# Kernel optimization log

Hardware: AMD Instinct MI355X
Metric: run time of the kernel (lower is better)

## Reference

```python
import jax, jax.numpy as jnp
import numpy as np

N = 8192
TEMP = 0.5
EPS = 1e-12


def _normalize(z):
    # F.normalize(z, p=2, dim=1): x / max(||x||, eps)
    n = jnp.sqrt(jnp.sum(z * z, axis=1, keepdims=True))
    return z / jnp.maximum(n, EPS)


def _gcn(edge_index, edge_weight, x, w, b):
    # torch.sparse.mm(adj, x @ w): out[row] += adj[row, col] * support[col]
    support = x @ w
    msg = support[edge_index[1]] * edge_weight[:, None]
    return jax.ops.segment_sum(msg, edge_index[0], num_segments=N) + b


def _encoder(edge_index, edge_weight, feat, w_l1a, b_l1a, w_l1b, b_l1b, w_g1, b_g1, w_g2, b_g2):
    x = jax.nn.relu(feat @ w_l1a + b_l1a) @ w_l1b + b_l1b  # [N, 32]
    h = jax.nn.relu(_gcn(edge_index, edge_weight, x, w_g1, b_g1))  # [N, hid]
    return _gcn(edge_index, edge_weight, h, w_g2, b_g2)  # [N, act_fn]


def _proj(h, w_fc1, b_fc1, w_fc2, b_fc2):
    return jax.nn.elu(h @ w_fc1 + b_fc1) @ w_fc2 + b_fc2


def _loss(z1, z2):
    z1n = _normalize(z1)
    z2n = _normalize(z2)
    refl = jnp.exp((z1n @ z1n.T) / TEMP)      # [N, N]
    between = jnp.exp((z1n @ z2n.T) / TEMP)   # [N, N]
    denom = refl.sum(1) + between.sum(1) - jnp.diagonal(refl)
    return -jnp.log(jnp.diagonal(between) / denom)


def setup_inputs() -> dict:
    key = jax.random.key(0)
    ks = jax.random.split(key, 20)
    E = 262144
    in_dim, hid_dim, act_fn, out_dim = 512, 256, 128, 64

    def kaiming(k, shape):
        fan_in = shape[0]
        bound = np.sqrt(6.0 / fan_in)
        return jax.random.uniform(k, shape, jnp.float32, -bound, bound)

    return {
        "feat1": jax.random.normal(ks[0], (N, in_dim), jnp.float32),
        "feat2": jax.random.normal(ks[1], (N, in_dim), jnp.float32),
        "edge_index1": jax.random.randint(ks[2], (2, E), 0, N, jnp.int32),
        "edge_weight1": jax.random.uniform(ks[3], (E,), jnp.float32),
        "edge_index2": jax.random.randint(ks[4], (2, E), 0, N, jnp.int32),
        "edge_weight2": jax.random.uniform(ks[5], (E,), jnp.float32),
        "w_l1a": kaiming(ks[6], (in_dim, 64)),
        "b_l1a": jnp.zeros((64,), jnp.float32),
        "w_l1b": kaiming(ks[7], (64, 32)),
        "b_l1b": jnp.zeros((32,), jnp.float32),
        "w_g1": kaiming(ks[8], (32, hid_dim)),
        "b_g1": jnp.zeros((hid_dim,), jnp.float32),
        "w_g2": kaiming(ks[9], (hid_dim, act_fn)),
        "b_g2": jnp.zeros((act_fn,), jnp.float32),
        "w_fc1": kaiming(ks[10], (act_fn, out_dim)),
        "b_fc1": jnp.zeros((out_dim,), jnp.float32),
        "w_fc2": kaiming(ks[11], (out_dim, act_fn)),
        "b_fc2": jnp.zeros((act_fn,), jnp.float32),
    }


def reference(feat1, feat2, edge_index1, edge_weight1, edge_index2, edge_weight2,
              w_l1a, b_l1a, w_l1b, b_l1b, w_g1, b_g1, w_g2, b_g2,
              w_fc1, b_fc1, w_fc2, b_fc2):
    h1 = _encoder(edge_index1, edge_weight1, feat1, w_l1a, b_l1a, w_l1b, b_l1b, w_g1, b_g1, w_g2, b_g2)
    h2 = _encoder(edge_index2, edge_weight2, feat2, w_l1a, b_l1a, w_l1b, b_l1b, w_g1, b_g1, w_g2, b_g2)
    z1 = _proj(h1, w_fc1, b_fc1, w_fc2, b_fc2)
    z2 = _proj(h2, w_fc1, b_fc1, w_fc2, b_fc2)
    l1 = _loss(z1, z2)
    l2 = _loss(z2, z1)
    return ((l1 + l2) * 0.5).mean()
```

## Files before the change

### kernel.cpp

```cpp
#include <hip/hip_runtime.h>
#include <hip/hip_bf16.h>
#include <math.h>


#define NROWS 8192
#define MROWS 16384
#define NEDGE 262144

typedef __attribute__((ext_vector_type(8))) short bf16x8;
typedef __attribute__((ext_vector_type(4))) float f32x4;
typedef __attribute__((ext_vector_type(2))) float f32x2;
typedef __attribute__((ext_vector_type(8))) int i32x8;
typedef long long i64;

__device__ __forceinline__ short f2bf(float f){
  union { float f; unsigned u; } cv; cv.f = f;
  unsigned u = cv.u;
  unsigned r = (u + 0x7fffu + ((u >> 16) & 1u)) >> 16;
  return (short)r;
}
__device__ __forceinline__ f32x4 mfma16(bf16x8 a, bf16x8 b, f32x4 c){
  return __builtin_amdgcn_mfma_f32_16x16x32_bf16(a, b, c, 0, 0, 0);
}
__device__ __forceinline__ float fexp2(float x){
#if __has_builtin(__builtin_amdgcn_exp2f)
  return __builtin_amdgcn_exp2f(x);
#else
  return exp2f(x);
#endif
}

template<int CTRL>
__device__ __forceinline__ float dpp_add(float v){
  int s = __builtin_amdgcn_update_dpp(0, __builtin_bit_cast(int, v),
                                      CTRL, 0xf, 0xf, true);
  return v + __builtin_bit_cast(float, s);
}
__device__ __forceinline__ float red16(float v){
  v = dpp_add<0x101>(v);
  v = dpp_add<0x102>(v);
  v = dpp_add<0x104>(v);
  v = dpp_add<0x108>(v);
  return v;
}

__device__ unsigned char f2e4m3_sw(float f){
  float a = fabsf(f);
  unsigned s = (__float_as_uint(f)>>24)&0x80u;
  if (!(a>0.f)) return (unsigned char)s;
  if (a>448.f) a=448.f;
  int e; frexpf(a,&e);
  int eff=e-1;
  unsigned code;
  if (eff<-6){
    float q=rintf(a*512.f);
    code=(unsigned)q; if(code>7)code=7;
  } else {
    float q=rintf(a*exp2f((float)(3-eff)));
    unsigned mant=(unsigned)q;
    if(mant>=16){mant=8;eff++;}
    if(eff>8) return (unsigned char)(s|0x7e);
    code=((unsigned)(eff+7)<<3)|(mant-8);
  }
  return (unsigned char)(s|code);
}
__device__ __forceinline__ unsigned short pack2fp8(float a, float b){
#if __has_builtin(__builtin_amdgcn_cvt_pk_fp8_f32)
  int v = __builtin_amdgcn_cvt_pk_fp8_f32(a, b, 0, false);
  return (unsigned short)(v & 0xffff);
#else
  return (unsigned short)((unsigned)f2e4m3_sw(a) | ((unsigned)f2e4m3_sw(b)<<8));
#endif
}

struct WtArgs {
  const float* src[6];
  short* dst[6];
  int K[6], N[6];
  int off[7];
  int nwt;
};
__global__ void setup_k(WtArgs a, const int* __restrict__ ei1, const int* __restrict__ ei2,
                        int* __restrict__ deg1, int* __restrict__ deg2){
  int b = blockIdx.x;
  if (b < a.nwt){
    int i = b*256 + threadIdx.x;
    if (i >= a.off[6]) return;
    int s = 0;
    #pragma unroll
    for (int j=1;j<6;j++) if (i >= a.off[j]) s=j;
    int l = i - a.off[s];
    int K=a.K[s], N=a.N[s];
    int k=l/N, n=l-k*N;
    a.dst[s][(long)n*K+k] = f2bf(a.src[s][l]);
  } else {
    int hb = b - a.nwt;
    const int* ei = (hb < NEDGE/256) ? ei1 : ei2;
    int* deg = (hb < NEDGE/256) ? deg1 : deg2;
    int e = (hb % (NEDGE/256))*256 + threadIdx.x;
    atomicAdd(&deg[ei[e]], 1);
  }
}

__global__ __launch_bounds__(256) void mlp12_k(const float* __restrict__ F0, const float* __restrict__ F1,
                                               const short* __restrict__ Wa, const float* __restrict__ ba,
                                               const short* __restrict__ Wb, const float* __restrict__ bb,
                                               short* __restrict__ xb){
  __shared__ short As[32*520];
  __shared__ short a1s[32*72];
  const int tid = threadIdx.x;
  const int m0 = blockIdx.x*32;
  const float* F = (m0 < NROWS) ? (F0 + (long)m0*512) : (F1 + (long)(m0-NROWS)*512);
  {
    float4 st[16];
    #pragma unroll
    for (int i=0;i<16;i++) st[i] = *(const float4*)(F + (long)(i*256+tid)*4);
    #pragma unroll
    for (int i=0;i<16;i++){
      int idx = i*256+tid, row = idx>>7, c4 = idx&127;
      unsigned lo = (unsigned)(unsigned short)f2bf(st[i].x) | ((unsigned)(unsigned short)f2bf(st[i].y)<<16);
      unsigned hi = (unsigned)(unsigned short)f2bf(st[i].z) | ((unsigned)(unsigned short)f2bf(st[i].w)<<16);
      uint2 o = {lo, hi};
      *(uint2*)&As[row*520 + c4*4] = o;
    }
  }
  __syncthreads();
  const int wave = tid>>6, lane = tid&63, quad = lane>>4, cl = lane&15;
  f32x4 zero = {0.f,0.f,0.f,0.f};
  {
    const int wno = wave*16;
    f32x4 acc[2] = {zero, zero};
    #pragma unroll
    for (int kc=0;kc<16;kc++){
      const int ko = kc*32 + quad*8;
      bf16x8 a0 = *(const bf16x8*)&As[(cl)*520 + ko];
      bf16x8 a1 = *(const bf16x8*)&As[(16+cl)*520 + ko];
      bf16x8 b = *(const bf16x8*)(Wa + (long)(wno + cl)*512 + ko);
      acc[0] = mfma16(a0, b, acc[0]);
      acc[1] = mfma16(a1, b, acc[1]);
    }
    int col = wno + cl;
    float bv = ba[col];
    #pragma unroll
    for (int mt=0;mt<2;mt++)
      #pragma unroll
      for (int r=0;r<4;r++)
        a1s[(mt*16 + quad*4 + r)*72 + col] = f2bf(fmaxf(acc[mt][r] + bv, 0.f));
  }
  __syncthreads();
  if (wave < 2){
    f32x4 acc2[2] = {zero, zero};
    #pragma unroll
    for (int kc=0;kc<2;kc++){
      const int ko = kc*32 + quad*8;
      bf16x8 a = *(const bf16x8*)&a1s[(wave*16+cl)*72 + ko];
      #pragma unroll
      for (int nt=0;nt<2;nt++){
        bf16x8 b = *(const bf16x8*)(Wb + (long)(nt*16 + cl)*64 + ko);
        acc2[nt] = mfma16(a, b, acc2[nt]);
      }
    }
    #pragma unroll
    for (int nt=0;nt<2;nt++){
      int col = nt*16 + cl;
      float bv = bb[col];
      #pragma unroll
      for (int r=0;r<4;r++)
        xb[(long)(m0 + wave*16 + quad*4 + r)*32 + col] = f2bf(acc2[nt][r] + bv);
    }
  }
}

__global__ void scan2_k(const int* __restrict__ deg1, int* __restrict__ rs1, int* __restrict__ cur1,
                        const int* __restrict__ deg2, int* __restrict__ rs2, int* __restrict__ cur2){
  const int* deg = blockIdx.x ? deg2 : deg1;
  int* rowstart = blockIdx.x ? rs2 : rs1;
  int* cursor = blockIdx.x ? cur2 : cur1;
  __shared__ int csum[256];
  int t = threadIdx.x;
  int loc[32];
  int s = 0;
  for (int j=0;j<32;j++){ int d = deg[t*32+j]; loc[j] = s; s += d; }
  int v = s;
  csum[t] = v;
  __syncthreads();
  for (int st=1; st<256; st<<=1){
    int o = (t >= st) ? csum[t-st] : 0;
    __syncthreads();
    v += o;
    csum[t] = v;
    __syncthreads();
  }
  int base = v - s;
  for (int j=0;j<32;j++){ int w = base + loc[j]; rowstart[t*32+j]=w; cursor[t*32+j]=w; }
  if (t==255) rowstart[NROWS] = v;
}
__global__ void fill2_k(const int* __restrict__ ei1, const float* __restrict__ w1, int* __restrict__ cur1,
                        int* __restrict__ ecol1, float* __restrict__ ew1,
                        const int* __restrict__ ei2, const float* __restrict__ w2, int* __restrict__ cur2,
                        int* __restrict__ ecol2, float* __restrict__ ew2){
  int b = blockIdx.x;
  bool g2 = (b >= NEDGE/256);
  const int* ei = g2 ? ei2 : ei1;
  const float* w = g2 ? w2 : w1;
  int* cursor = g2 ? cur2 : cur1;
  int* ecol = g2 ? ecol2 : ecol1;
  float* ew = g2 ? ew2 : ew1;
  int e = (b % (NEDGE/256))*256 + threadIdx.x;
  int r = ei[e];
  int p = atomicAdd(&cursor[r], 1);
  ecol[p] = ei[NEDGE + e];
  ew[p] = w[e];
}

__device__ __forceinline__ void acc8(float* acc, int4 v, float f){
  const unsigned* u = (const unsigned*)&v;
  #pragma unroll
  for (int i=0;i<4;i++){
    union{unsigned x; float y;} lo, hi;
    lo.x = u[i] << 16;
    hi.x = u[i] & 0xffff0000u;
    acc[2*i]   = fmaf(f, lo.y, acc[2*i]);
    acc[2*i+1] = fmaf(f, hi.y, acc[2*i+1]);
  }
}
template<int C>
__device__ __forceinline__ void gather_row(float* acc, const short* sb,
                                           const int* ec, const float* w, int s, int e){
  int k = s;
  for (; k+16 <= e; k+=16){
    int c[16]; float f[16]; int4 v[16];
    #pragma unroll
    for (int u=0;u<16;u++){ c[u]=ec[k+u]; f[u]=w[k+u]; }
    #pragma unroll
    for (int u=0;u<16;u++) v[u] = *(const int4*)(sb + (long)c[u]*C);
    #pragma unroll
    for (int u=0;u<16;u++) acc8(acc, v[u], f[u]);
  }
  for (; k+4 <= e; k+=4){
    int c0=ec[k],c1=ec[k+1],c2=ec[k+2],c3=ec[k+3];
    float f0=w[k],f1=w[k+1],f2=w[k+2],f3=w[k+3];
    int4 v0 = *(const int4*)(sb + (long)c0*C);
    int4 v1 = *(const int4*)(sb + (long)c1*C);
    int4 v2 = *(const int4*)(sb + (long)c2*C);
    int4 v3 = *(const int4*)(sb + (long)c3*C);
    acc8(acc,v0,f0); acc8(acc,v1,f1); acc8(acc,v2,f2); acc8(acc,v3,f3);
  }
  for (; k < e; k++){
    int4 v0 = *(const int4*)(sb + (long)ec[k]*C);
    acc8(acc,v0,w[k]);
  }
}

template<int C, bool RELU, bool HASB>
__global__ __launch_bounds__(256) void gather_k(const short* __restrict__ sup,
    const int* __restrict__ rs1, const int* __restrict__ ec1, const float* __restrict__ w1,
    const int* __restrict__ rs2, const int* __restrict__ ec2, const float* __restrict__ w2,
    const float* __restrict__ bias, short* __restrict__ out){
  constexpr int G = C/8;
  const int g = threadIdx.x % G;
  const int sub = threadIdx.x / G;
  const int row = blockIdx.x*(256/G) + sub;
  const int* rs; const int* ec; const float* w; int soff, lr;
  if (row < NROWS){ rs=rs1; ec=ec1; w=w1; soff=0; lr=row; }
  else            { rs=rs2; ec=ec2; w=w2; soff=NROWS; lr=row-NROWS; }
  const short* sb = sup + (long)soff*C + g*8;
  float acc[8];
  #pragma unroll
  for (int j=0;j<8;j++) acc[j] = HASB ? bias[g*8+j] : 0.f;
  gather_row<C>(acc, sb, ec, w, rs[lr], rs[lr+1]);
  int4 ov;
  unsigned* ou = (unsigned*)&ov;
  #pragma unroll
  for (int i=0;i<4;i++){
    float a0 = acc[2*i], a1 = acc[2*i+1];
    if (RELU){ a0 = fmaxf(a0,0.f); a1 = fmaxf(a1,0.f); }
    ou[i] = (unsigned)(unsigned short)f2bf(a0) | ((unsigned)(unsigned short)f2bf(a1)<<16);
  }
  *(int4*)(out + (long)row*C + g*8) = ov;
}

__global__ __launch_bounds__(256) void gg_k(const short* __restrict__ xb,
    const int* __restrict__ rs1, const int* __restrict__ ec1, const float* __restrict__ w1,
    const int* __restrict__ rs2, const int* __restrict__ ec2, const float* __restrict__ w2,
    const short* __restrict__ Wg1, const float* __restrict__ bg1,
    const short* __restrict__ Wg2, short* __restrict__ s2){
  __shared__ short axs[64*40];
  __shared__ short hbs[64*264];
  const int tid = threadIdx.x;
  const int m0 = blockIdx.x*64;
  {
    const int g = tid & 3, sub = tid >> 2;
    const int row = m0 + sub;
    const int* rs; const int* ec; const float* w; int soff, lr;
    if (row < NROWS){ rs=rs1; ec=ec1; w=w1; soff=0; lr=row; }
    else            { rs=rs2; ec=ec2; w=w2; soff=NROWS; lr=row-NROWS; }
    const short* sb = xb + (long)soff*32 + g*8;
    float acc[8];
    #pragma unroll
    for (int j=0;j<8;j++) acc[j] = 0.f;
    gather_row<32>(acc, sb, ec, w, rs[lr], rs[lr+1]);
    int4 ov;
    unsigned* ou = (unsigned*)&ov;
    #pragma unroll
    for (int i=0;i<4;i++)
      ou[i] = (unsigned)(unsigned short)f2bf(acc[2*i]) | ((unsigned)(unsigned short)f2bf(acc[2*i+1])<<16);
    *(int4*)&axs[sub*40 + g*8] = ov;
  }
  __syncthreads();
  const int wave = tid>>6, lane = tid&63, quad = lane>>4, cl = lane&15;
  f32x4 zero = {0.f,0.f,0.f,0.f};
  {
    const int wno = wave*64;
    f32x4 acc[4][4];
    #pragma unroll
    for (int i=0;i<4;i++)
      #pragma unroll
      for (int j=0;j<4;j++) acc[i][j]=zero;
    const int ko = quad*8;
    bf16x8 a[4], b[4];
    #pragma unroll
    for (int mt=0;mt<4;mt++)
      a[mt] = *(const bf16x8*)&axs[(mt*16+cl)*40 + ko];
    #pragma unroll
    for (int nt=0;nt<4;nt++)
      b[nt] = *(const bf16x8*)(Wg1 + (long)(wno + nt*16 + cl)*32 + ko);
    #pragma unroll
    for (int mt=0;mt<4;mt++)
      #pragma unroll
      for (int nt=0;nt<4;nt++)
        acc[mt][nt] = mfma16(a[mt], b[nt], acc[mt][nt]);
    #pragma unroll
    for (int nt=0;nt<4;nt++){
      int col = wno + nt*16 + cl;
      float bv = bg1[col];
      #pragma unroll
      for (int mt=0;mt<4;mt++)
        #pragma unroll
        for (int r=0;r<4;r++)
          hbs[(mt*16 + quad*4 + r)*264 + col] = f2bf(fmaxf(acc[mt][nt][r] + bv, 0.f));
    }
  }
  __syncthreads();
  {
    const int wno = wave*32;
    f32x4 acc[4][2];
    #pragma unroll
    for (int i=0;i<4;i++){ acc[i][0]=zero; acc[i][1]=zero; }
    #pragma unroll
    for (int kc=0;kc<8;kc++){
      const int ko = kc*32 + quad*8;
      bf16x8 a[4], b[2];
      #pragma unroll
      for (int mt=0;mt<4;mt++)
        a[mt] = *(const bf16x8*)&hbs[(mt*16+cl)*264 + ko];
      #pragma unroll
      for (int nt=0;nt<2;nt++)
        b[nt] = *(const bf16x8*)(Wg2 + (long)(wno + nt*16 + cl)*256 + ko);
      #pragma unroll
      for (int mt=0;mt<4;mt++)
        #pragma unroll
        for (int nt=0;nt<2;nt++)
          acc[mt][nt] = mfma16(a[mt], b[nt], acc[mt][nt]);
    }
    #pragma unroll
    for (int mt=0;mt<4;mt++)
      #pragma unroll
      for (int nt=0;nt<2;nt++){
        int col = wno + nt*16 + cl;
        #pragma unroll
        for (int r=0;r<4;r++)
          s2[(long)(m0 + mt*16 + quad*4 + r)*128 + col] = f2bf(acc[mt][nt][r]);
      }
  }
}

__global__ __launch_bounds__(256) void pn_k(const short* __restrict__ hh,
    const short* __restrict__ Wf1, const float* __restrict__ bf1,
    const short* __restrict__ Wf2, const float* __restrict__ bf2,
    unsigned short* __restrict__ Zf, float* __restrict__ bdot){
  __shared__ short hs[64*136];
  __shared__ short t2s[64*72];
  __shared__ float zs[64*132];
  __shared__ float sp[4][64];
  __shared__ float dp[4][32];
  __shared__ float rnS[64];
  const float SQKE = 1.6986436f;
  const int tid = threadIdx.x;
  const int wave = tid>>6, lane = tid&63, quad = lane>>4, cl = lane&15;
  const int m0h = blockIdx.x*32;
  {
    const short* r1 = hh + (long)m0h*128;
    const short* r2 = hh + (long)(NROWS + m0h)*128;
    #pragma unroll
    for (int i=0;i<2;i++){
      int idx = i*256 + tid;
      int row = idx >> 4, c16 = idx & 15;
      *(int4*)&hs[row*136 + c16*8] = *(const int4*)(r1 + row*128 + c16*8);
      *(int4*)&hs[(32+row)*136 + c16*8] = *(const int4*)(r2 + row*128 + c16*8);
    }
  }
  __syncthreads();
  f32x4 zero = {0.f,0.f,0.f,0.f};
  {
    const int wno = wave*16;
    f32x4 acc[4];
    #pragma unroll
    for (int i=0;i<4;i++) acc[i]=zero;
    #pragma unroll
    for (int kc=0;kc<4;kc++){
      const int ko = kc*32 + quad*8;
      bf16x8 a[4], b;
      #pragma unroll
      for (int mt=0;mt<4;mt++)
        a[mt] = *(const bf16x8*)&hs[(mt*16+cl)*136 + ko];
      b = *(const bf16x8*)(Wf1 + (long)(wno + cl)*128 + ko);
      #pragma unroll
      for (int mt=0;mt<4;mt++) acc[mt] = mfma16(a[mt], b, acc[mt]);
    }
    int col = wno + cl;
    float bv = bf1[col];
    #pragma unroll
    for (int mt=0;mt<4;mt++)
      #pragma unroll
      for (int r=0;r<4;r++){
        float v = acc[mt][r] + bv;
        v = (v > 0.f) ? v : expm1f(v);
        t2s[(mt*16 + quad*4 + r)*72 + col] = f2bf(v);
      }
  }
  __syncthreads();
  {
    const int wno = wave*32;
    f32x4 acc[4][2];
    #pragma unroll
    for (int i=0;i<4;i++){ acc[i][0]=zero; acc[i][1]=zero; }
    #pragma unroll
    for (int kc=0;kc<2;kc++){
      const int ko = kc*32 + quad*8;
      bf16x8 a[4], b[2];
      #pragma unroll
      for (int mt=0;mt<4;mt++)
        a[mt] = *(const bf16x8*)&t2s[(mt*16+cl)*72 + ko];
      #pragma unroll
      for (int nt=0;nt<2;nt++)
        b[nt] = *(const bf16x8*)(Wf2 + (long)(wno + nt*16 + cl)*64 + ko);
      #pragma unroll
      for (int mt=0;mt<4;mt++)
        #pragma unroll
        for (int nt=0;nt<2;nt++)
          acc[mt][nt] = mfma16(a[mt], b[nt], acc[mt][nt]);
    }
    #pragma unroll
    for (int mt=0;mt<4;mt++)
      #pragma unroll
      for (int nt=0;nt<2;nt++){
        int col = wno + nt*16 + cl;
        float bv = bf2[col];
        #pragma unroll
        for (int r=0;r<4;r++)
          zs[(mt*16 + quad*4 + r)*132 + col] = acc[mt][nt][r] + bv;
      }
  }
  __syncthreads();
  {
    int row = tid & 63, qtr = tid >> 6;
    const float* zr = &zs[row*132 + qtr*32];
    float s = 0.f;
    #pragma unroll 8
    for (int c=0;c<32;c++) s += zr[c]*zr[c];
    sp[qtr][row] = s;
    if (row < 32){
      const float* zb_ = &zs[(row+32)*132 + qtr*32];
      float d = 0.f;
      #pragma unroll 8
      for (int c=0;c<32;c++) d += zr[c]*zb_[c];
      dp[qtr][row] = d;
    }
  }
  __syncthreads();
  if (tid < 64){
    float ssq = sp[0][tid]+sp[1][tid]+sp[2][tid]+sp[3][tid];
    rnS[tid] = 1.f / fmaxf(sqrtf(ssq), 1e-12f);
  }
  __syncthreads();
  if (tid < 32){
    float dot = dp[0][tid]+dp[1][tid]+dp[2][tid]+dp[3][tid];
    bdot[m0h + tid] = dot * rnS[tid] * rnS[tid+32];
  }
  {
    int lr = tid >> 2;
    int grow = (lr < 32) ? (m0h + lr) : (NROWS + m0h + lr - 32);
    float s = rnS[lr] * SQKE;
    int p0 = (tid & 3)*16;
    long gbase = (long)(grow>>4)*1024 + (long)(grow&15)*16 + (long)(p0>>4)*256;
    #pragma unroll
    for (int pp=0;pp<16;pp++){
      int p = p0 + pp;
      Zf[gbase + pp] = pack2fp8(zs[lr*132 + 2*p]*s, zs[lr*132 + 2*p + 1]*s);
    }
  }
}

__global__ __launch_bounds__(256,4) void gram3_k(const unsigned char* __restrict__ Zf,
                                                 float* __restrict__ P){
  __shared__ float srow[4][64];
  __shared__ float scol[4][64];
  const int wave = threadIdx.x>>6, lane = threadIdx.x&63;
  const int t = blockIdx.x*4 + wave;
  int ti = (int)((513.0f - sqrtf(513.0f*513.0f - 8.0f*(float)t))*0.5f);
  while ((ti+1)*256 - ((ti+1)*ti)/2 <= t) ti++;
  while (ti*256 - (ti*(ti-1))/2 > t) ti--;
  const int tj = ti + (t - (ti*256 - (ti*(ti-1))/2));
  const unsigned char* za = Zf + (long)ti*8192 + lane*32;
  const unsigned char* zb = Zf + (long)tj*8192 + lane*32;
  const int quad = lane>>4, cl = lane&15;

  f32x4 zero = {0.f,0.f,0.f,0.f};
  f32x2 z2 = {0.f,0.f};
  f32x2 cs[4] = {z2,z2,z2,z2};

  i32x8 Bf[4];
  #pragma unroll
  for (int nt=0;nt<4;nt++)
    Bf[nt] = *(const i32x8*)(zb + nt*2048);

  i32x8 Ab[2];
  Ab[0] = *(const i32x8*)(za);
  Ab[1] = *(const i32x8*)(za + 2048);

  auto exprow = [&](const f32x4* ar, int mt){
    f32x2 r01 = z2, r23 = z2;
    #pragma unroll
    for (int nt=0;nt<4;nt++){
      f32x4 v = ar[nt];
      float e0 = fexp2(v[0]), e1 = fexp2(v[1]);
      float e2 = fexp2(v[2]), e3 = fexp2(v[3]);
      f32x2 p01 = {e0,e1}, p23 = {e2,e3};
      r01 += p01; r23 += p23;
      cs[nt] += p01; cs[nt] += p23;
    }
    float s0 = red16(r01.x);
    float s1 = red16(r01.y);
    float s2 = red16(r23.x);
    float s3 = red16(r23.y);
    if (cl==0){
      f32x4 rv = {s0, s1, s2, s3};
      *(f32x4*)&srow[wave][mt*16 + quad*4] = rv;
    }
  };

  const int SC1 = 0x7F;
  f32x4 acc2[2][4];
  #pragma unroll
  for (int nt=0;nt<4;nt++)
    acc2[0][nt] = __builtin_amdgcn_mfma_scale_f32_16x16x128_f8f6f4(
        Ab[0], Bf[nt], zero, 0, 0, 0, SC1, 0, SC1);
  #pragma unroll
  for (int mt=1; mt<4; mt++){
    const int cur = mt&1, prv = cur^1;
    if (mt<3)
      Ab[prv] = *(const i32x8*)(za + (mt+1)*2048);
    #pragma unroll
    for (int nt=0;nt<4;nt++)
      acc2[cur][nt] = __builtin_amdgcn_mfma_scale_f32_16x16x128_f8f6f4(
          Ab[cur], Bf[nt], zero, 0, 0, 0, SC1, 0, SC1);
    exprow(&acc2[prv][0], mt-1);
  }
  exprow(&acc2[1][0], 3);

  __threadfence_block();
  P[((long)ti*256 + tj)*64 + lane] = srow[wave][lane];
  if (ti != tj){
    #pragma unroll
    for (int nt=0;nt<4;nt++){
      float s = cs[nt].x + cs[nt].y;
      s += __shfl_xor(s,16); s += __shfl_xor(s,32);
      if (quad==0) scol[wave][nt*16 + cl] = s;
    }
    __threadfence_block();
    P[((long)tj*256 + ti)*64 + lane] = scol[wave][lane];
  }
}

__global__ void rloss_k(const float* __restrict__ P, const float* __restrict__ bdot,
                        float* __restrict__ out){
  __shared__ float red[256];
  const float E2 = 7.3890560989306495f;
  int t = threadIdx.x;
  int i = blockIdx.x*256 + t;
  int j = i + NROWS;
  const float* p1 = P + (long)(i>>6)*256*64 + (i&63);
  const float* p2 = P + (long)(j>>6)*256*64 + (j&63);
  float s1 = 0.f, s2 = 0.f;
  #pragma unroll 8
  for (int b=0;b<256;b++){ s1 += p1[b*64]; s2 += p2[b*64]; }
  float lb = 2.f * bdot[i];
  float term = 0.5f * ((logf(s1 - E2) - lb) + (logf(s2 - E2) - lb));
  red[t]=term; __syncthreads();
  for (int st=128; st>0; st>>=1){ if (t<st) red[t]+=red[t+st]; __syncthreads(); }
  if (t==0) atomicAdd(out, red[0] / (float)NROWS);
}

extern "C" void kernel_launch(void* const* d_in, const int* in_sizes, int n_in,
                              void* d_out, int out_size, void* d_ws, size_t ws_size,
                              hipStream_t stream){
  const float* feat1 = (const float*)d_in[0];
  const float* feat2 = (const float*)d_in[1];
  const int*   ei1   = (const int*)d_in[2];
  const float* w1    = (const float*)d_in[3];
  const int*   ei2   = (const int*)d_in[4];
  const float* w2    = (const float*)d_in[5];
  const float* w_l1a = (const float*)d_in[6];
  const float* b_l1a = (const float*)d_in[7];
  const float* w_l1b = (const float*)d_in[8];
  const float* b_l1b = (const float*)d_in[9];
  const float* w_g1  = (const float*)d_in[10];
  const float* b_g1  = (const float*)d_in[11];
  const float* w_g2  = (const float*)d_in[12];
  const float* b_g2  = (const float*)d_in[13];
  const float* w_fc1 = (const float*)d_in[14];
  const float* b_fc1 = (const float*)d_in[15];
  const float* w_fc2 = (const float*)d_in[16];
  const float* b_fc2 = (const float*)d_in[17];

  float* P = (float*)d_ws;
  char* base = (char*)d_ws;
  size_t off = (size_t)17<<20;
  auto alloc = [&](size_t bytes)->void*{
    void* r = base + off;
    off = (off + bytes + 255) & ~(size_t)255;
    return r;
  };
  short* xb   = (short*)alloc((size_t)MROWS*32*2);
  short* s2   = (short*)alloc((size_t)MROWS*128*2);
  short* hh   = (short*)alloc((size_t)MROWS*128*2);
  short* wl1a_t = (short*)alloc(512*64*2);
  short* wl1b_t = (short*)alloc(64*32*2);
  short* wg1_t  = (short*)alloc(32*256*2);
  short* wg2_t  = (short*)alloc(256*128*2);
  short* wfc1_t = (short*)alloc(128*64*2);
  short* wfc2_t = (short*)alloc(64*128*2);
  unsigned short* Zf = (unsigned short*)alloc((size_t)MROWS*128);
  int*   deg1 = (int*)alloc(NROWS*4);
  int*   deg2 = (int*)alloc(NROWS*4);
  int* rs1  = (int*)alloc((NROWS+1)*4);
  int* cur1 = (int*)alloc(NROWS*4);
  int* rs2  = (int*)alloc((NROWS+1)*4);
  int* cur2 = (int*)alloc(NROWS*4);
  int*   ecol1 = (int*)alloc((size_t)NEDGE*4);
  float* ewt1  = (float*)alloc((size_t)NEDGE*4);
  int*   ecol2 = (int*)alloc((size_t)NEDGE*4);
  float* ewt2  = (float*)alloc((size_t)NEDGE*4);
  float* bdot  = (float*)alloc(NROWS*4);

  hipMemsetAsync(deg1, 0, (size_t)2*NROWS*4, stream);
  hipMemsetAsync(d_out, 0, sizeof(float), stream);

  WtArgs wa;
  wa.src[0]=w_l1a; wa.dst[0]=wl1a_t; wa.K[0]=512; wa.N[0]=64;
  wa.src[1]=w_l1b; wa.dst[1]=wl1b_t; wa.K[1]=64;  wa.N[1]=32;
  wa.src[2]=w_g1;  wa.dst[2]=wg1_t;  wa.K[2]=32;  wa.N[2]=256;
  wa.src[3]=w_g2;  wa.dst[3]=wg2_t;  wa.K[3]=256; wa.N[3]=128;
  wa.src[4]=w_fc1; wa.dst[4]=wfc1_t; wa.K[4]=128; wa.N[4]=64;
  wa.src[5]=w_fc2; wa.dst[5]=wfc2_t; wa.K[5]=64;  wa.N[5]=128;
  wa.off[0]=0;
  for (int i=0;i<6;i++) wa.off[i+1] = wa.off[i] + wa.K[i]*wa.N[i];
  wa.nwt = (wa.off[6]+255)/256;

  setup_k<<<wa.nwt + 2*(NEDGE/256),256,0,stream>>>(wa, ei1, ei2, deg1, deg2);
  scan2_k<<<2,256,0,stream>>>(deg1, rs1, cur1, deg2, rs2, cur2);
  fill2_k<<<2*(NEDGE/256),256,0,stream>>>(ei1, w1, cur1, ecol1, ewt1,
                                          ei2, w2, cur2, ecol2, ewt2);

  mlp12_k<<<MROWS/32,256,0,stream>>>(feat1, feat2, wl1a_t, b_l1a, wl1b_t, b_l1b, xb);
  gg_k<<<MROWS/64,256,0,stream>>>(xb, rs1,ecol1,ewt1, rs2,ecol2,ewt2,
                                  wg1_t, b_g1, wg2_t, s2);
  gather_k<128,false,true><<<MROWS/16,256,0,stream>>>(s2, rs1,ecol1,ewt1,
                                                      rs2,ecol2,ewt2, b_g2, hh);
  pn_k<<<NROWS/32,256,0,stream>>>(hh, wfc1_t, b_fc1, wfc2_t, b_fc2, Zf, bdot);

  gram3_k<<<8224,256,0,stream>>>((const unsigned char*)Zf, P);
  rloss_k<<<NROWS/256,256,0,stream>>>(P, bdot, (float*)d_out);
}
```

Measured before the change: 254.4 us.

## Fuse CSR fill with MLP, fold second GCN gather into projection, parallelize loss reduce

Three changes. The CSR fill kernel and the input MLP now run as one launch, with the two kinds of work split by block index, so they can overlap and one launch disappears. The second GCN gather is moved into the projection kernel, which gathers rows directly into shared memory, so the intermediate hh buffer and its round trip through memory go away. The final loss reduction runs on 256 blocks instead of 32, splitting the 256-term partial sums across 8 thread groups. Risks: the projection kernel now has fewer blocks, 256, doing the gather, so gather parallelism drops, and the gather has irregular latency.

```diff
diff --git a/kernel.cpp b/kernel.cpp
--- a/kernel.cpp
+++ b/kernel.cpp
@@ -102,75 +102,6 @@
   }
 }
 
-__global__ __launch_bounds__(256) void mlp12_k(const float* __restrict__ F0, const float* __restrict__ F1,
-                                               const short* __restrict__ Wa, const float* __restrict__ ba,
-                                               const short* __restrict__ Wb, const float* __restrict__ bb,
-                                               short* __restrict__ xb){
-  __shared__ short As[32*520];
-  __shared__ short a1s[32*72];
-  const int tid = threadIdx.x;
-  const int m0 = blockIdx.x*32;
-  const float* F = (m0 < NROWS) ? (F0 + (long)m0*512) : (F1 + (long)(m0-NROWS)*512);
-  {
-    float4 st[16];
-    #pragma unroll
-    for (int i=0;i<16;i++) st[i] = *(const float4*)(F + (long)(i*256+tid)*4);
-    #pragma unroll
-    for (int i=0;i<16;i++){
-      int idx = i*256+tid, row = idx>>7, c4 = idx&127;
-      unsigned lo = (unsigned)(unsigned short)f2bf(st[i].x) | ((unsigned)(unsigned short)f2bf(st[i].y)<<16);
-      unsigned hi = (unsigned)(unsigned short)f2bf(st[i].z) | ((unsigned)(unsigned short)f2bf(st[i].w)<<16);
-      uint2 o = {lo, hi};
-      *(uint2*)&As[row*520 + c4*4] = o;
-    }
-  }
-  __syncthreads();
-  const int wave = tid>>6, lane = tid&63, quad = lane>>4, cl = lane&15;
-  f32x4 zero = {0.f,0.f,0.f,0.f};
-  {
-    const int wno = wave*16;
-    f32x4 acc[2] = {zero, zero};
-    #pragma unroll
-    for (int kc=0;kc<16;kc++){
-      const int ko = kc*32 + quad*8;
-      bf16x8 a0 = *(const bf16x8*)&As[(cl)*520 + ko];
-      bf16x8 a1 = *(const bf16x8*)&As[(16+cl)*520 + ko];
-      bf16x8 b = *(const bf16x8*)(Wa + (long)(wno + cl)*512 + ko);
-      acc[0] = mfma16(a0, b, acc[0]);
-      acc[1] = mfma16(a1, b, acc[1]);
-    }
-    int col = wno + cl;
-    float bv = ba[col];
-    #pragma unroll
-    for (int mt=0;mt<2;mt++)
-      #pragma unroll
-      for (int r=0;r<4;r++)
-        a1s[(mt*16 + quad*4 + r)*72 + col] = f2bf(fmaxf(acc[mt][r] + bv, 0.f));
-  }
-  __syncthreads();
-  if (wave < 2){
-    f32x4 acc2[2] = {zero, zero};
-    #pragma unroll
-    for (int kc=0;kc<2;kc++){
-      const int ko = kc*32 + quad*8;
-      bf16x8 a = *(const bf16x8*)&a1s[(wave*16+cl)*72 + ko];
-      #pragma unroll
-      for (int nt=0;nt<2;nt++){
-        bf16x8 b = *(const bf16x8*)(Wb + (long)(nt*16 + cl)*64 + ko);
-        acc2[nt] = mfma16(a, b, acc2[nt]);
-      }
-    }
-    #pragma unroll
-    for (int nt=0;nt<2;nt++){
-      int col = nt*16 + cl;
-      float bv = bb[col];
-      #pragma unroll
-      for (int r=0;r<4;r++)
-        xb[(long)(m0 + wave*16 + quad*4 + r)*32 + col] = f2bf(acc2[nt][r] + bv);
-    }
-  }
-}
-
 __global__ void scan2_k(const int* __restrict__ deg1, int* __restrict__ rs1, int* __restrict__ cur1,
                         const int* __restrict__ deg2, int* __restrict__ rs2, int* __restrict__ cur2){
   const int* deg = blockIdx.x ? deg2 : deg1;
@@ -195,22 +126,92 @@
   for (int j=0;j<32;j++){ int w = base + loc[j]; rowstart[t*32+j]=w; cursor[t*32+j]=w; }
   if (t==255) rowstart[NROWS] = v;
 }
-__global__ void fill2_k(const int* __restrict__ ei1, const float* __restrict__ w1, int* __restrict__ cur1,
-                        int* __restrict__ ecol1, float* __restrict__ ew1,
-                        const int* __restrict__ ei2, const float* __restrict__ w2, int* __restrict__ cur2,
-                        int* __restrict__ ecol2, float* __restrict__ ew2){
-  int b = blockIdx.x;
-  bool g2 = (b >= NEDGE/256);
-  const int* ei = g2 ? ei2 : ei1;
-  const float* w = g2 ? w2 : w1;
-  int* cursor = g2 ? cur2 : cur1;
-  int* ecol = g2 ? ecol2 : ecol1;
-  float* ew = g2 ? ew2 : ew1;
-  int e = (b % (NEDGE/256))*256 + threadIdx.x;
-  int r = ei[e];
-  int p = atomicAdd(&cursor[r], 1);
-  ecol[p] = ei[NEDGE + e];
-  ew[p] = w[e];
+
+__global__ __launch_bounds__(256) void fm_k(const float* __restrict__ F0, const float* __restrict__ F1,
+    const short* __restrict__ Wa, const float* __restrict__ ba,
+    const short* __restrict__ Wb, const float* __restrict__ bb, short* __restrict__ xb,
+    const int* __restrict__ ei1, const float* __restrict__ w1, int* __restrict__ cur1,
+    int* __restrict__ ecol1, float* __restrict__ ew1,
+    const int* __restrict__ ei2, const float* __restrict__ w2, int* __restrict__ cur2,
+    int* __restrict__ ecol2, float* __restrict__ ew2){
+  __shared__ short As[32*520];
+  __shared__ short a1s[32*72];
+  const int tid = threadIdx.x;
+  if (blockIdx.x >= MROWS/32){
+    int b = blockIdx.x - MROWS/32;
+    bool g2 = (b >= NEDGE/256);
+    const int* ei = g2 ? ei2 : ei1;
+    const float* w = g2 ? w2 : w1;
+    int* cursor = g2 ? cur2 : cur1;
+    int* ecol = g2 ? ecol2 : ecol1;
+    float* ew = g2 ? ew2 : ew1;
+    int e = (b % (NEDGE/256))*256 + tid;
+    int r = ei[e];
+    int p = atomicAdd(&cursor[r], 1);
+    ecol[p] = ei[NEDGE + e];
+    ew[p] = w[e];
+    return;
+  }
+  const int m0 = blockIdx.x*32;
+  const float* F = (m0 < NROWS) ? (F0 + (long)m0*512) : (F1 + (long)(m0-NROWS)*512);
+  {
+    float4 st[16];
+    #pragma unroll
+    for (int i=0;i<16;i++) st[i] = *(const float4*)(F + (long)(i*256+tid)*4);
+    #pragma unroll
+    for (int i=0;i<16;i++){
+      int idx = i*256+tid, row = idx>>7, c4 = idx&127;
+      unsigned lo = (unsigned)(unsigned short)f2bf(st[i].x) | ((unsigned)(unsigned short)f2bf(st[i].y)<<16);
+      unsigned hi = (unsigned)(unsigned short)f2bf(st[i].z) | ((unsigned)(unsigned short)f2bf(st[i].w)<<16);
+      uint2 o = {lo, hi};
+      *(uint2*)&As[row*520 + c4*4] = o;
+    }
+  }
+  __syncthreads();
+  const int wave = tid>>6, lane = tid&63, quad = lane>>4, cl = lane&15;
+  f32x4 zero = {0.f,0.f,0.f,0.f};
+  {
+    const int wno = wave*16;
+    f32x4 acc[2] = {zero, zero};
+    #pragma unroll
+    for (int kc=0;kc<16;kc++){
+      const int ko = kc*32 + quad*8;
+      bf16x8 a0 = *(const bf16x8*)&As[(cl)*520 + ko];
+      bf16x8 a1 = *(const bf16x8*)&As[(16+cl)*520 + ko];
+      bf16x8 b = *(const bf16x8*)(Wa + (long)(wno + cl)*512 + ko);
+      acc[0] = mfma16(a0, b, acc[0]);
+      acc[1] = mfma16(a1, b, acc[1]);
+    }
+    int col = wno + cl;
+    float bv = ba[col];
+    #pragma unroll
+    for (int mt=0;mt<2;mt++)
+      #pragma unroll
+      for (int r=0;r<4;r++)
+        a1s[(mt*16 + quad*4 + r)*72 + col] = f2bf(fmaxf(acc[mt][r] + bv, 0.f));
+  }
+  __syncthreads();
+  if (wave < 2){
+    f32x4 acc2[2] = {zero, zero};
+    #pragma unroll
+    for (int kc=0;kc<2;kc++){
+      const int ko = kc*32 + quad*8;
+      bf16x8 a = *(const bf16x8*)&a1s[(wave*16+cl)*72 + ko];
+      #pragma unroll
+      for (int nt=0;nt<2;nt++){
+        bf16x8 b = *(const bf16x8*)(Wb + (long)(nt*16 + cl)*64 + ko);
+        acc2[nt] = mfma16(a, b, acc2[nt]);
+      }
+    }
+    #pragma unroll
+    for (int nt=0;nt<2;nt++){
+      int col = nt*16 + cl;
+      float bv = bb[col];
+      #pragma unroll
+      for (int r=0;r<4;r++)
+        xb[(long)(m0 + wave*16 + quad*4 + r)*32 + col] = f2bf(acc2[nt][r] + bv);
+    }
+  }
 }
 
 __device__ __forceinline__ void acc8(float* acc, int4 v, float f){
@@ -252,34 +253,6 @@
   }
 }
 
-template<int C, bool RELU, bool HASB>
-__global__ __launch_bounds__(256) void gather_k(const short* __restrict__ sup,
-    const int* __restrict__ rs1, const int* __restrict__ ec1, const float* __restrict__ w1,
-    const int* __restrict__ rs2, const int* __restrict__ ec2, const float* __restrict__ w2,
-    const float* __restrict__ bias, short* __restrict__ out){
-  constexpr int G = C/8;
-  const int g = threadIdx.x % G;
-  const int sub = threadIdx.x / G;
-  const int row = blockIdx.x*(256/G) + sub;
-  const int* rs; const int* ec; const float* w; int soff, lr;
-  if (row < NROWS){ rs=rs1; ec=ec1; w=w1; soff=0; lr=row; }
-  else            { rs=rs2; ec=ec2; w=w2; soff=NROWS; lr=row-NROWS; }
-  const short* sb = sup + (long)soff*C + g*8;
-  float acc[8];
-  #pragma unroll
-  for (int j=0;j<8;j++) acc[j] = HASB ? bias[g*8+j] : 0.f;
-  gather_row<C>(acc, sb, ec, w, rs[lr], rs[lr+1]);
-  int4 ov;
-  unsigned* ou = (unsigned*)&ov;
-  #pragma unroll
-  for (int i=0;i<4;i++){
-    float a0 = acc[2*i], a1 = acc[2*i+1];
-    if (RELU){ a0 = fmaxf(a0,0.f); a1 = fmaxf(a1,0.f); }
-    ou[i] = (unsigned)(unsigned short)f2bf(a0) | ((unsigned)(unsigned short)f2bf(a1)<<16);
-  }
-  *(int4*)(out + (long)row*C + g*8) = ov;
-}
-
 __global__ __launch_bounds__(256) void gg_k(const short* __restrict__ xb,
     const int* __restrict__ rs1, const int* __restrict__ ec1, const float* __restrict__ w1,
     const int* __restrict__ rs2, const int* __restrict__ ec2, const float* __restrict__ w2,
@@ -375,7 +348,10 @@
   }
 }
 
-__global__ __launch_bounds__(256) void pn_k(const short* __restrict__ hh,
+__global__ __launch_bounds__(256) void pn_k(const short* __restrict__ s2,
+    const int* __restrict__ rs1, const int* __restrict__ ec1, const float* __restrict__ w1,
+    const int* __restrict__ rs2, const int* __restrict__ ec2, const float* __restrict__ w2,
+    const float* __restrict__ bg2,
     const short* __restrict__ Wf1, const float* __restrict__ bf1,
     const short* __restrict__ Wf2, const float* __restrict__ bf2,
     unsigned short* __restrict__ Zf, float* __restrict__ bdot){
@@ -390,14 +366,25 @@
   const int wave = tid>>6, lane = tid&63, quad = lane>>4, cl = lane&15;
   const int m0h = blockIdx.x*32;
   {
-    const short* r1 = hh + (long)m0h*128;
-    const short* r2 = hh + (long)(NROWS + m0h)*128;
-    #pragma unroll
-    for (int i=0;i<2;i++){
-      int idx = i*256 + tid;
-      int row = idx >> 4, c16 = idx & 15;
-      *(int4*)&hs[row*136 + c16*8] = *(const int4*)(r1 + row*128 + c16*8);
-      *(int4*)&hs[(32+row)*136 + c16*8] = *(const int4*)(r2 + row*128 + c16*8);
+    const int g = tid & 15, sub = tid >> 4;
+    #pragma unroll 1
+    for (int pass=0; pass<4; pass++){
+      int hrow = pass*16 + sub;
+      int lr = m0h + (hrow & 31);
+      const int* rs; const int* ec; const float* w; long soff;
+      if (hrow < 32){ rs=rs1; ec=ec1; w=w1; soff=0; }
+      else          { rs=rs2; ec=ec2; w=w2; soff=NROWS; }
+      const short* sb = s2 + soff*128 + g*8;
+      float acc[8];
+      #pragma unroll
+      for (int j=0;j<8;j++) acc[j] = bg2[g*8+j];
+      gather_row<128>(acc, sb, ec, w, rs[lr], rs[lr+1]);
+      int4 ov;
+      unsigned* ou = (unsigned*)&ov;
+      #pragma unroll
+      for (int i=0;i<4;i++)
+        ou[i] = (unsigned)(unsigned short)f2bf(acc[2*i]) | ((unsigned)(unsigned short)f2bf(acc[2*i+1])<<16);
+      *(int4*)&hs[hrow*136 + g*8] = ov;
     }
   }
   __syncthreads();
@@ -583,23 +570,37 @@
   }
 }
 
-__global__ void rloss_k(const float* __restrict__ P, const float* __restrict__ bdot,
-                        float* __restrict__ out){
-  __shared__ float red[256];
+__global__ __launch_bounds__(256) void rloss_k(const float* __restrict__ P,
+                                               const float* __restrict__ bdot,
+                                               float* __restrict__ out){
+  __shared__ float ps[8][32][2];
   const float E2 = 7.3890560989306495f;
   int t = threadIdx.x;
-  int i = blockIdx.x*256 + t;
+  int rloc = t & 31, grp = t >> 5;
+  int i = blockIdx.x*32 + rloc;
   int j = i + NROWS;
-  const float* p1 = P + (long)(i>>6)*256*64 + (i&63);
-  const float* p2 = P + (long)(j>>6)*256*64 + (j&63);
+  const float* p1 = P + (long)(i>>6)*256*64 + (long)grp*32*64 + (i&63);
+  const float* p2 = P + (long)(j>>6)*256*64 + (long)grp*32*64 + (j&63);
   float s1 = 0.f, s2 = 0.f;
   #pragma unroll 8
-  for (int b=0;b<256;b++){ s1 += p1[b*64]; s2 += p2[b*64]; }
-  float lb = 2.f * bdot[i];
-  float term = 0.5f * ((logf(s1 - E2) - lb) + (logf(s2 - E2) - lb));
-  red[t]=term; __syncthreads();
-  for (int st=128; st>0; st>>=1){ if (t<st) red[t]+=red[t+st]; __syncthreads(); }
-  if (t==0) atomicAdd(out, red[0] / (float)NROWS);
+  for (int b=0;b<32;b++){ s1 += p1[b*64]; s2 += p2[b*64]; }
+  ps[grp][rloc][0] = s1;
+  ps[grp][rloc][1] = s2;
+  __syncthreads();
+  if (t < 64){
+    float term = 0.f;
+    if (t < 32){
+      float a1 = 0.f, a2 = 0.f;
+      #pragma unroll
+      for (int g=0; g<8; g++){ a1 += ps[g][t][0]; a2 += ps[g][t][1]; }
+      int ii = blockIdx.x*32 + t;
+      float lb = 2.f * bdot[ii];
+      term = 0.5f * ((logf(a1 - E2) - lb) + (logf(a2 - E2) - lb));
+    }
+    #pragma unroll
+    for (int m=1; m<64; m<<=1) term += __shfl_xor(term, m);
+    if (t==0) atomicAdd(out, term / (float)NROWS);
+  }
 }
 
 extern "C" void kernel_launch(void* const* d_in, const int* in_sizes, int n_in,
@@ -634,7 +635,6 @@
   };
   short* xb   = (short*)alloc((size_t)MROWS*32*2);
   short* s2   = (short*)alloc((size_t)MROWS*128*2);
-  short* hh   = (short*)alloc((size_t)MROWS*128*2);
   short* wl1a_t = (short*)alloc(512*64*2);
   short* wl1b_t = (short*)alloc(64*32*2);
   short* wg1_t  = (short*)alloc(32*256*2);
@@ -670,16 +670,14 @@
 
   setup_k<<<wa.nwt + 2*(NEDGE/256),256,0,stream>>>(wa, ei1, ei2, deg1, deg2);
   scan2_k<<<2,256,0,stream>>>(deg1, rs1, cur1, deg2, rs2, cur2);
-  fill2_k<<<2*(NEDGE/256),256,0,stream>>>(ei1, w1, cur1, ecol1, ewt1,
-                                          ei2, w2, cur2, ecol2, ewt2);
-
-  mlp12_k<<<MROWS/32,256,0,stream>>>(feat1, feat2, wl1a_t, b_l1a, wl1b_t, b_l1b, xb);
+  fm_k<<<MROWS/32 + 2*(NEDGE/256),256,0,stream>>>(feat1, feat2, wl1a_t, b_l1a,
+      wl1b_t, b_l1b, xb,
+      ei1, w1, cur1, ecol1, ewt1,
+      ei2, w2, cur2, ecol2, ewt2);
   gg_k<<<MROWS/64,256,0,stream>>>(xb, rs1,ecol1,ewt1, rs2,ecol2,ewt2,
                                   wg1_t, b_g1, wg2_t, s2);
-  gather_k<128,false,true><<<MROWS/16,256,0,stream>>>(s2, rs1,ecol1,ewt1,
-                                                      rs2,ecol2,ewt2, b_g2, hh);
-  pn_k<<<NROWS/32,256,0,stream>>>(hh, wfc1_t, b_fc1, wfc2_t, b_fc2, Zf, bdot);
-
+  pn_k<<<NROWS/32,256,0,stream>>>(s2, rs1,ecol1,ewt1, rs2,ecol2,ewt2, b_g2,
+                                  wfc1_t, b_fc1, wfc2_t, b_fc2, Zf, bdot);
   gram3_k<<<8224,256,0,stream>>>((const unsigned char*)Zf, P);
-  rloss_k<<<NROWS/256,256,0,stream>>>(P, bdot, (float*)d_out);
-}
+  rloss_k<<<NROWS/32,256,0,stream>>>(P, bdot, (float*)d_out);
+}
```

Measured after the change: 247.6 us, median of 2. -2.7%, faster.
